# Performance work log

Hardware: AMD Instinct MI355X
Metric: run time of the kernel (lower is better)

The kernel has to match this reference:

```python
import jax, jax.numpy as jnp
import numpy as np

B, N, D = 1, 1024, 3584
H, KVH, HD = 28, 4, 128
I = 18944
SEC = [16, 24, 24]  # mrope_section, sums to HD//2
EPS_RMS = 1e-6
EPS_SM = 1e-6


def setup_inputs() -> dict:
    key = jax.random.key(0)
    ks = jax.random.split(key, 16)
    s = 0.02
    return {
        "hidden_states": jax.random.normal(ks[0], (B, N, D), jnp.float32),
        "cos": jax.random.uniform(ks[1], (3, B, N, HD), jnp.float32, -1.0, 1.0),
        "sin": jax.random.uniform(ks[2], (3, B, N, HD), jnp.float32, -1.0, 1.0),
        "prune_mask": jax.random.randint(ks[3], (B, N), 0, 2, jnp.int32),
        "Wq": jax.random.normal(ks[4], (D, H * HD), jnp.float32) * s,
        "bq": jnp.zeros((H * HD,), jnp.float32),
        "Wk": jax.random.normal(ks[5], (D, KVH * HD), jnp.float32) * s,
        "bk": jnp.zeros((KVH * HD,), jnp.float32),
        "Wv": jax.random.normal(ks[6], (D, KVH * HD), jnp.float32) * s,
        "bv": jnp.zeros((KVH * HD,), jnp.float32),
        "Wo": jax.random.normal(ks[7], (H * HD, D), jnp.float32) * s,
        "ln1_w": jnp.ones((D,), jnp.float32),
        "ln2_w": jnp.ones((D,), jnp.float32),
        "Wg": jax.random.normal(ks[8], (D, I), jnp.float32) * s,
        "Wu": jax.random.normal(ks[9], (D, I), jnp.float32) * s,
        "Wd": jax.random.normal(ks[10], (I, D), jnp.float32) * s,
    }


def _rmsnorm(x, w):
    v = jnp.mean(x * x, axis=-1, keepdims=True)
    return x * jax.lax.rsqrt(v + EPS_RMS) * w


def _rotate_half(x):
    h = x.shape[-1] // 2
    return jnp.concatenate([-x[..., h:], x[..., :h]], axis=-1)


def _mrope_select(t):
    # t: (3, B, N, HD) -> (B, 1, N, HD), picking section i from axis i%3
    parts, idx = [], 0
    for i, s in enumerate(SEC * 2):
        parts.append(t[i % 3, :, :, idx:idx + s])
        idx += s
    return jnp.concatenate(parts, axis=-1)[:, None]


def reference(hidden_states, cos, sin, prune_mask, Wq, bq, Wk, bk, Wv, bv, Wo,
              ln1_w, ln2_w, Wg, Wu, Wd):
    x = _rmsnorm(hidden_states, ln1_w)
    q = (x @ Wq + bq).reshape(B, N, H, HD).transpose(0, 2, 1, 3)
    k = (x @ Wk + bk).reshape(B, N, KVH, HD).transpose(0, 2, 1, 3)
    v = (x @ Wv + bv).reshape(B, N, KVH, HD).transpose(0, 2, 1, 3)

    cf, sf = _mrope_select(cos), _mrope_select(sin)
    q = q * cf + _rotate_half(q) * sf
    k = k * cf + _rotate_half(k) * sf

    groups = H // KVH
    k = jnp.repeat(k, groups, axis=1)  # (B,H,N,HD)
    v = jnp.repeat(v, groups, axis=1)

    scores = jnp.einsum("bhqd,bhkd->bhqk", q, k) / np.sqrt(HD).astype(np.float32)
    causal = jnp.tril(jnp.ones((N, N), bool))
    scores = jnp.where(causal, scores, jnp.float32(-1e9))

    # custom prune-masked softmax (softmax_with_mask)
    am = prune_mask.astype(jnp.float32)[:, None, None, :]  # (B,1,1,N)
    eye = jnp.eye(N, dtype=jnp.float32)
    am = am + (1.0 - am) * eye
    mx = jnp.max(scores, axis=-1, keepdims=True)
    e = jnp.exp(scores - mx) * am
    attn = (e + EPS_SM / N) / (jnp.sum(e, axis=-1, keepdims=True) + EPS_SM)

    o = jnp.einsum("bhqk,bhkd->bhqd", attn, v)
    o = o.transpose(0, 2, 1, 3).reshape(B, N, H * HD) @ Wo

    h = hidden_states + o
    y = _rmsnorm(h, ln2_w)
    mlp = (jax.nn.silu(y @ Wg) * (y @ Wu)) @ Wd
    return h + mlp
```

## Files before the change

### kernel.cpp

```cpp
#include <hip/hip_runtime.h>
#include <hip/hip_bf16.h>


#define SEQ   1024
#define DIM   3584
#define NH    28
#define NKVH  4
#define HDIM  128
#define IDIM  18944
#define QKVN  4608
#define GUN   37888

typedef __attribute__((ext_vector_type(8))) __bf16 bf16x8;
typedef __attribute__((ext_vector_type(4))) __bf16 bf16x4;
typedef __attribute__((ext_vector_type(4))) float  f32x4;

static constexpr size_t OFF_WQKVT = 0;
static constexpr size_t OFF_WOT   = OFF_WQKVT + (size_t)QKVN*DIM*2;
static constexpr size_t OFF_WGUT  = OFF_WOT   + (size_t)DIM*DIM*2;
static constexpr size_t OFF_WDT   = OFF_WGUT  + (size_t)GUN*DIM*2;
static constexpr size_t OFF_XB    = OFF_WDT   + (size_t)DIM*IDIM*2;
static constexpr size_t OFF_QKV   = OFF_XB    + (size_t)SEQ*DIM*2;
static constexpr size_t OFF_VT    = OFF_QKV   + (size_t)SEQ*QKVN*2;
static constexpr size_t OFF_VSUMP = OFF_VT    + (size_t)NKVH*HDIM*SEQ*2;
static constexpr size_t OFF_VSUM  = OFF_VSUMP + 4*8*128*4;
static constexpr size_t OFF_BQKV  = OFF_VSUM  + 4*128*4;
static constexpr size_t OFF_OB    = OFF_BQKV  + (size_t)QKVN*4;
static constexpr size_t OFF_HB    = OFF_OB    + (size_t)SEQ*DIM*2;
static constexpr size_t OFF_YB    = OFF_HB    + (size_t)SEQ*DIM*4;
static constexpr size_t OFF_GU    = OFF_YB    + (size_t)SEQ*DIM*2;
static constexpr size_t OFF_PB    = OFF_GU    + (size_t)SEQ*GUN*2;
static constexpr size_t OFF_PART  = OFF_GU;
static constexpr size_t OFF_CTR   = OFF_VSUMP;

#define GLL16(gp, lp)                                                        \
  __builtin_amdgcn_global_load_lds(                                         \
      (const __attribute__((address_space(1))) void*)(gp),                  \
      (__attribute__((address_space(3))) void*)(lp), 16, 0, 0)

#define BAR    asm volatile("s_barrier" ::: "memory")
#define LGKM0  asm volatile("s_waitcnt lgkmcnt(0)" ::: "memory")
#define VM4    asm volatile("s_waitcnt vmcnt(4)" ::: "memory")

__global__ __launch_bounds__(256) void transconv_kernel(
    const float* __restrict__ W, __bf16* __restrict__ WT, int K, int N, int mode)
{
  __shared__ __bf16 t[64][72];
  const int tid = threadIdx.x;
  const int k0 = blockIdx.y * 64, n0 = blockIdx.x * 64;
#pragma unroll
  for (int it = 0; it < 4; ++it) {
    int idx = it * 256 + tid;
    int r = idx >> 4, c4 = idx & 15;
    float4 v = *(const float4*)(W + (size_t)(k0 + r) * N + n0 + c4 * 4);
    t[r][c4 * 4 + 0] = (__bf16)v.x;
    t[r][c4 * 4 + 1] = (__bf16)v.y;
    t[r][c4 * 4 + 2] = (__bf16)v.z;
    t[r][c4 * 4 + 3] = (__bf16)v.w;
  }
  __syncthreads();
#pragma unroll
  for (int it = 0; it < 2; ++it) {
    int idx = it * 256 + tid;
    int r = idx >> 3, c8 = idx & 7;
    bf16x8 o;
#pragma unroll
    for (int i = 0; i < 8; ++i) o[i] = t[c8 * 8 + i][r];
    const int nlog = n0 + r;
    const int orow = (mode == 0) ? nlog
                   : ((nlog >> 4) << 5) + ((mode == 2) ? 16 : 0) + (nlog & 15);
    *(bf16x8*)(WT + (size_t)orow * K + k0 + c8 * 8) = o;
  }
}

__global__ __launch_bounds__(256) void pack_bias_kernel(
    const float* __restrict__ bq, const float* __restrict__ bk,
    const float* __restrict__ bv, float* __restrict__ out)
{
  int i = blockIdx.x * 256 + threadIdx.x;
  if (i < DIM) out[i] = bq[i];
  else if (i < DIM + 512) out[i] = bk[i - DIM];
  else if (i < QKVN) out[i] = bv[i - DIM - 512];
}

__global__ __launch_bounds__(256) void rmsnorm_kernel(
    const float* __restrict__ in, const float* __restrict__ w,
    __bf16* __restrict__ out)
{
  const int row = blockIdx.x;
  const int t = threadIdx.x;
  const float* x = in + (size_t)row * DIM;
  float4 v[4];
  float ss = 0.f;
#pragma unroll
  for (int i = 0; i < 4; ++i) {
    int idx = t + i * 256;
    if (idx < 896) {
      v[i] = ((const float4*)x)[idx];
      ss += v[i].x * v[i].x + v[i].y * v[i].y + v[i].z * v[i].z + v[i].w * v[i].w;
    }
  }
#pragma unroll
  for (int m = 1; m < 64; m <<= 1) ss += __shfl_xor(ss, m);
  __shared__ float red[4];
  if ((t & 63) == 0) red[t >> 6] = ss;
  __syncthreads();
  float tot = red[0] + red[1] + red[2] + red[3];
  float rs = rsqrtf(tot / (float)DIM + 1e-6f);
#pragma unroll
  for (int i = 0; i < 4; ++i) {
    int idx = t + i * 256;
    if (idx < 896) {
      float4 wv = ((const float4*)w)[idx];
      bf16x4 o;
      o[0] = (__bf16)(v[i].x * rs * wv.x);
      o[1] = (__bf16)(v[i].y * rs * wv.y);
      o[2] = (__bf16)(v[i].z * rs * wv.z);
      o[3] = (__bf16)(v[i].w * rs * wv.w);
      *(bf16x4*)(out + (size_t)row * DIM + idx * 4) = o;
    }
  }
}

template<int S, bool BF16OUT, bool BIAS>
__global__ __launch_bounds__(256) void reduce_kernel(
    const float* __restrict__ part, const float* __restrict__ resid,
    const float* __restrict__ bias, void* __restrict__ out, int N, int MN4)
{
  const int i4 = blockIdx.x * 256 + threadIdx.x;
  if (i4 >= MN4) return;
  const size_t base = (size_t)i4 * 4;
  f32x4 s = *(const f32x4*)(part + base);
#pragma unroll
  for (int k = 1; k < S; ++k)
    s += *(const f32x4*)(part + (size_t)k * MN4 * 4 + base);
  if (BIAS) {
    const int col = (int)(base % N);
    s += *(const f32x4*)(bias + col);
  }
  if (resid != nullptr) s += *(const f32x4*)(resid + base);
  if (BF16OUT) {
    bf16x4 o;
#pragma unroll
    for (int j = 0; j < 4; ++j) o[j] = (__bf16)s[j];
    *(bf16x4*)((__bf16*)out + base) = o;
  } else {
    *(f32x4*)((float*)out + base) = s;
  }
}

__global__ __launch_bounds__(256) void reduce_rms_kernel(
    const float* __restrict__ part, const float* __restrict__ resid,
    const float* __restrict__ w, float* __restrict__ hout,
    __bf16* __restrict__ yout, int* __restrict__ ctr)
{
  const int row = blockIdx.x;
  const int t = threadIdx.x;
  if (row == 0 && t == 0) atomicExch(ctr, 0);
  const size_t base = (size_t)row * DIM;
  const size_t slab = (size_t)SEQ * DIM;
  f32x4 v[4];
  float ss = 0.f;
#pragma unroll
  for (int i = 0; i < 4; ++i) {
    int idx = t + i * 256;
    if (idx < 896) {
      f32x4 s = *(const f32x4*)(part + base + idx * 4);
      s += *(const f32x4*)(part + slab + base + idx * 4);
      s += *(const f32x4*)(part + 2 * slab + base + idx * 4);
      s += *(const f32x4*)(part + 3 * slab + base + idx * 4);
      s += *(const f32x4*)(resid + base + idx * 4);
      v[i] = s;
      ss += s[0] * s[0] + s[1] * s[1] + s[2] * s[2] + s[3] * s[3];
      *(f32x4*)(hout + base + idx * 4) = s;
    }
  }
#pragma unroll
  for (int m = 1; m < 64; m <<= 1) ss += __shfl_xor(ss, m);
  __shared__ float red[4];
  if ((t & 63) == 0) red[t >> 6] = ss;
  __syncthreads();
  float tot = red[0] + red[1] + red[2] + red[3];
  float rs = rsqrtf(tot / (float)DIM + 1e-6f);
#pragma unroll
  for (int i = 0; i < 4; ++i) {
    int idx = t + i * 256;
    if (idx < 896) {
      f32x4 wv = *(const f32x4*)(w + idx * 4);
      bf16x4 o;
#pragma unroll
      for (int j = 0; j < 4; ++j) o[j] = (__bf16)(v[i][j] * rs * wv[j]);
      *(bf16x4*)(yout + base + idx * 4) = o;
    }
  }
}

template<int EPI, int PERSIST>
__global__ __launch_bounds__(512, 1) void gemm256_kernel(
    const __bf16* __restrict__ A, const __bf16* __restrict__ BT,
    void* __restrict__ OUT, int M, int N, int K, int Kc, int gridY,
    int NT, int* __restrict__ ctr)
{
  __shared__ int4 lds4[8192];
  __shared__ int s_t;
  char* ldsc = (char*)lds4;
  const int tid = threadIdx.x;
  const int l = tid & 63, w = tid >> 6;
  const int wr = w >> 2, wc = w & 3;
  const int lg = l >> 4, lc = l & 15;

  int cdst[2], crow[2], cslot[2];
#pragma unroll
  for (int j = 0; j < 2; ++j) {
    const int c = (j * 8 + w) * 64 + l;
    crow[j] = c >> 3;
    cslot[j] = (c & 7) ^ (crow[j] & 7);
    cdst[j] = (j * 8 + w) * 1024;
  }
  const int sw = lc & 7;
  const int rdA = (wr * 128 + lc) * 128;
  const int rdB = 32768 + (wc * 64 + lc) * 128;
  const int sk0 = (lg ^ sw) * 16;
  const int sk1 = ((4 | lg) ^ sw) * 16;
  const int ntn = N >> 8;

  for (;;) {
    int tw;
    if (PERSIST) {
      if (tid == 0) s_t = atomicAdd(ctr, 1);
      __syncthreads();
      tw = s_t;
      if (tw >= NT) return;
    } else {
      const int nwg = gridDim.x;
      const int bq8 = nwg >> 3, br8 = nwg & 7;
      const int xcd = blockIdx.x & 7, bidx = blockIdx.x >> 3;
      tw = (xcd < br8 ? xcd * (bq8 + 1) : br8 * (bq8 + 1) + (xcd - br8) * bq8) + bidx;
    }
    const int wg2 = tw / gridY;
    const int row0 = (tw % gridY) * 256;
    const int col0 = (wg2 % ntn) * 256;
    const int ks_ = wg2 / ntn;
    const int kbase = ks_ * Kc;

    size_t aoffj[2], boffj[2];
    int dstj[2];
#pragma unroll
    for (int j = 0; j < 2; ++j) {
      aoffj[j] = (size_t)(row0 + crow[j]) * K + kbase + cslot[j] * 8;
      boffj[j] = (size_t)(col0 + crow[j]) * K + kbase + cslot[j] * 8;
      dstj[j] = cdst[j];
    }

#define STG_A(U, KT, BUFB) do {                                              \
    GLL16(A + aoffj[0] + (size_t)(U) * 128 * K + (size_t)(KT) * 64,          \
          ldsc + (BUFB) + (U) * 16384 + dstj[0]);                            \
    GLL16(A + aoffj[1] + (size_t)(U) * 128 * K + (size_t)(KT) * 64,          \
          ldsc + (BUFB) + (U) * 16384 + dstj[1]); } while (0)
#define STG_B(U, KT, BUFB) do {                                              \
    GLL16(BT + boffj[0] + (size_t)(U) * 128 * K + (size_t)(KT) * 64,         \
          ldsc + (BUFB) + 32768 + (U) * 16384 + dstj[0]);                    \
    GLL16(BT + boffj[1] + (size_t)(U) * 128 * K + (size_t)(KT) * 64,         \
          ldsc + (BUFB) + 32768 + (U) * 16384 + dstj[1]); } while (0)

    f32x4 acc[8][4] = {};
    bf16x8 af[4][2], bfr[4][2];

#define RD_A4(MH, BUFB) do { _Pragma("unroll")                               \
    for (int mm = 0; mm < 4; ++mm) {                                         \
      af[mm][0] = *(const bf16x8*)(ldsc + (BUFB) + rdA + ((MH) * 4 + mm) * 2048 + sk0); \
      af[mm][1] = *(const bf16x8*)(ldsc + (BUFB) + rdA + ((MH) * 4 + mm) * 2048 + sk1); } } while (0)
#define RD_B2(NL, BUFB) do { _Pragma("unroll")                               \
    for (int nn = 0; nn < 2; ++nn) {                                         \
      bfr[(NL) + nn][0] = *(const bf16x8*)(ldsc + (BUFB) + rdB + ((NL) + nn) * 2048 + sk0); \
      bfr[(NL) + nn][1] = *(const bf16x8*)(ldsc + (BUFB) + rdB + ((NL) + nn) * 2048 + sk1); } } while (0)

#define MFMA16(MH, NL) do { _Pragma("unroll")                                \
    for (int mm = 0; mm < 4; ++mm) { _Pragma("unroll")                       \
      for (int nn = 0; nn < 2; ++nn) {                                       \
        acc[(MH)*4+mm][(NL)+nn] = __builtin_amdgcn_mfma_f32_16x16x32_bf16(   \
            af[mm][0], bfr[(NL)+nn][0], acc[(MH)*4+mm][(NL)+nn], 0, 0, 0);   \
        acc[(MH)*4+mm][(NL)+nn] = __builtin_amdgcn_mfma_f32_16x16x32_bf16(   \
            af[mm][1], bfr[(NL)+nn][1], acc[(MH)*4+mm][(NL)+nn], 0, 0, 0); } } } while (0)

#define DO_MFMA(MH, NL)                                                      \
    __builtin_amdgcn_s_setprio(1); MFMA16(MH, NL);                           \
    __builtin_amdgcn_s_setprio(0)

    STG_B(0, 0, 0); STG_B(1, 0, 0); STG_A(0, 0, 0); STG_A(1, 0, 0);
    STG_B(0, 1, 65536); STG_B(1, 1, 65536);
    VM4;
    BAR;

    const int T = Kc >> 6;
#pragma unroll 1
    for (int i = 0; i < (T >> 1); ++i) {
      const int t1 = 2 * i + 1;
      const int se = (2 * i + 2 < T) ? 2 * i + 2 : 2 * i;
      const int so = (2 * i + 3 < T) ? 2 * i + 3 : t1;
      RD_A4(0, 0); RD_B2(0, 0); STG_A(0, t1, 65536);
      BAR; LGKM0; DO_MFMA(0, 0); BAR;
      RD_B2(2, 0); STG_A(1, t1, 65536);
      BAR; LGKM0; DO_MFMA(0, 2); BAR;
      RD_A4(1, 0); STG_B(0, se, 0);
      BAR; LGKM0; DO_MFMA(1, 2); BAR;
      STG_B(1, se, 0);
      VM4;
      BAR; DO_MFMA(1, 0); BAR;
      RD_A4(0, 65536); RD_B2(0, 65536); STG_A(0, se, 0);
      BAR; LGKM0; DO_MFMA(0, 0); BAR;
      RD_B2(2, 65536); STG_A(1, se, 0);
      BAR; LGKM0; DO_MFMA(0, 2); BAR;
      RD_A4(1, 65536); STG_B(0, so, 65536);
      BAR; LGKM0; DO_MFMA(1, 2); BAR;
      STG_B(1, so, 65536);
      VM4;
      BAR; DO_MFMA(1, 0); BAR;
    }
    asm volatile("s_waitcnt vmcnt(0)" ::: "memory");

    if (EPI == 0) {
      __bf16* PBo = (__bf16*)OUT;
      const int id = N >> 1;
      const int baseq = (col0 + wc * 64) >> 5;
#pragma unroll
      for (int m = 0; m < 8; ++m) {
#pragma unroll
        for (int p = 0; p < 2; ++p) {
          const int gcol = (baseq + p) * 16 + lc;
#pragma unroll
          for (int j = 0; j < 4; ++j) {
            const int row = row0 + wr * 128 + m * 16 + lg * 4 + j;
            const float g = acc[m][2 * p][j];
            const float u = acc[m][2 * p + 1][j];
            const float s = g / (1.f + __expf(-g));
            PBo[(size_t)row * id + gcol] = (__bf16)(s * u);
          }
        }
      }
    } else {
      float* P = (float*)OUT + (size_t)ks_ * M * N;
#pragma unroll
      for (int m = 0; m < 8; ++m)
#pragma unroll
        for (int n = 0; n < 4; ++n)
#pragma unroll
          for (int j = 0; j < 4; ++j)
            P[(size_t)(row0 + wr * 128 + m * 16 + lg * 4 + j) * N
              + (col0 + wc * 64 + n * 16 + lc)] = acc[m][n][j];
    }
    if (!PERSIST) return;
  }
#undef STG_A
#undef STG_B
#undef RD_A4
#undef RD_B2
#undef MFMA16
#undef DO_MFMA
}

__global__ __launch_bounds__(256) void rope_kernel(
    __bf16* __restrict__ qkv, const float* __restrict__ cosb,
    const float* __restrict__ sinb)
{
  const int n = blockIdx.x;
  for (int p = threadIdx.x; p < 32 * 64; p += 256) {
    const int head = p >> 6;
    const int d = p & 63;
    const int src = (d < 16) ? 0 : (d < 40) ? 1 : 2;
    const float* cb = cosb + (size_t)src * SEQ * HDIM + (size_t)n * HDIM;
    const float* sb = sinb + (size_t)src * SEQ * HDIM + (size_t)n * HDIM;
    const float c0 = cb[d], c1 = cb[d + 64];
    const float s0 = sb[d], s1 = sb[d + 64];
    const int col = (head < NH) ? head * HDIM : DIM + (head - NH) * HDIM;
    __bf16* q = qkv + (size_t)n * QKVN + col;
    const float a = (float)q[d];
    const float b = (float)q[d + 64];
    q[d]      = (__bf16)(a * c0 - b * s0);
    q[d + 64] = (__bf16)(b * c1 + a * s1);
  }
}

__global__ __launch_bounds__(256) void vtrans_kernel(
    const __bf16* __restrict__ qkv, __bf16* __restrict__ vT,
    float* __restrict__ vsump)
{
  __shared__ __bf16 t[128][132];
  const int nt = blockIdx.x, kvh = blockIdx.y;
  const int n0 = nt * 128;
  const int tid = threadIdx.x;
#pragma unroll
  for (int it = 0; it < 8; ++it) {
    int idx = it * 256 + tid;
    int nl = idx >> 4, c8 = idx & 15;
    bf16x8 v = *(const bf16x8*)(qkv + (size_t)(n0 + nl) * QKVN + 4096 + kvh * HDIM + c8 * 8);
#pragma unroll
    for (int i = 0; i < 8; ++i) t[nl][c8 * 8 + i] = v[i];
  }
  __syncthreads();
#pragma unroll
  for (int it = 0; it < 8; ++it) {
    int idx = it * 256 + tid;
    int d = idx >> 4, c8 = idx & 15;
    bf16x8 o;
#pragma unroll
    for (int i = 0; i < 8; ++i) o[i] = t[c8 * 8 + i][d];
    *(bf16x8*)(vT + (size_t)(kvh * HDIM + d) * SEQ + n0 + c8 * 8) = o;
  }
  if (tid < 128) {
    float s = 0.f;
    for (int nl = 0; nl < 128; ++nl) s += (float)t[nl][tid];
    vsump[(size_t)(kvh * 8 + nt) * 128 + tid] = s;
  }
}

__global__ __launch_bounds__(512) void vsum_reduce_kernel(
    const float* __restrict__ vsump, float* __restrict__ vsum)
{
  const int idx = threadIdx.x;
  const int kvh = idx >> 7, d = idx & 127;
  float s = 0.f;
#pragma unroll
  for (int nt = 0; nt < 8; ++nt) s += vsump[(size_t)(kvh * 8 + nt) * 128 + d];
  vsum[idx] = s;
}

__global__ __launch_bounds__(256) void attn_kernel(
    const __bf16* __restrict__ qkv, const __bf16* __restrict__ vT,
    const float* __restrict__ vsum, const int* __restrict__ prune,
    __bf16* __restrict__ o)
{
  __shared__ __bf16 plds[4 * 16 * 40];
  const int tid = threadIdx.x;
  const int l = tid & 63, w = tid >> 6;
  const int h = blockIdx.y;
  const int kvh = h / 7;
  const int qt = blockIdx.x;
  const int qbase = qt * 64 + w * 16;
  const int lg = l >> 4, lc = l & 15;
  __bf16* pw = plds + w * (16 * 40);

  bf16x8 qf[4];
#pragma unroll
  for (int s = 0; s < 4; ++s)
    qf[s] = *(const bf16x8*)(qkv + (size_t)(qbase + lc) * QKVN + h * HDIM + s * 32 + lg * 8);

  f32x4 oacc[8] = {};
  float mrun[4] = {-3e38f, -3e38f, -3e38f, -3e38f};
  float lrun[4] = {0.f, 0.f, 0.f, 0.f};

  const int kbEnd = ((qbase + 15) >> 5) + 1;
  for (int kb = 0; kb < kbEnd; ++kb) {
    f32x4 sacc[2] = {};
#pragma unroll
    for (int s = 0; s < 4; ++s) {
#pragma unroll
      for (int c = 0; c < 2; ++c) {
        bf16x8 kf = *(const bf16x8*)(qkv + (size_t)(kb * 32 + c * 16 + lc) * QKVN
                                     + DIM + kvh * HDIM + s * 32 + lg * 8);
        sacc[c] = __builtin_amdgcn_mfma_f32_16x16x32_bf16(qf[s], kf, sacc[c], 0, 0, 0);
      }
    }
    float p[2][4];
    int am[2];
#pragma unroll
    for (int c = 0; c < 2; ++c) {
      const int col = kb * 32 + c * 16 + lc;
      am[c] = (prune[col] != 0) ? 1 : 0;
#pragma unroll
      for (int j = 0; j < 4; ++j) {
        const int row = qbase + lg * 4 + j;
        float sv = sacc[c][j] * 0.08838834764831845f;
        p[c][j] = (col <= row) ? sv : -3e38f;
      }
    }
#pragma unroll
    for (int j = 0; j < 4; ++j) {
      float mx = fmaxf(p[0][j], p[1][j]);
      mx = fmaxf(mx, __shfl_xor(mx, 1));
      mx = fmaxf(mx, __shfl_xor(mx, 2));
      mx = fmaxf(mx, __shfl_xor(mx, 4));
      mx = fmaxf(mx, __shfl_xor(mx, 8));
      const float mnew = fmaxf(mrun[j], mx);
      const float scale = __expf(mrun[j] - mnew);
      mrun[j] = mnew;
      const int row = qbase + lg * 4 + j;
      float rs = 0.f;
#pragma unroll
      for (int c = 0; c < 2; ++c) {
        const int col = kb * 32 + c * 16 + lc;
        float e = __expf(p[c][j] - mnew);
        const int keep = (col == row) ? 1 : am[c];
        e = keep ? e : 0.f;
        p[c][j] = e;
        rs += e;
      }
      rs += __shfl_xor(rs, 1);
      rs += __shfl_xor(rs, 2);
      rs += __shfl_xor(rs, 4);
      rs += __shfl_xor(rs, 8);
      lrun[j] = lrun[j] * scale + rs;
#pragma unroll
      for (int df = 0; df < 8; ++df) oacc[df][j] *= scale;
    }
#pragma unroll
    for (int c = 0; c < 2; ++c)
#pragma unroll
      for (int j = 0; j < 4; ++j)
        pw[(lg * 4 + j) * 40 + c * 16 + lc] = (__bf16)p[c][j];
    bf16x8 pa = *(const bf16x8*)(pw + lc * 40 + lg * 8);
#pragma unroll
    for (int df = 0; df < 8; ++df) {
      bf16x8 vf = *(const bf16x8*)(vT + (size_t)(kvh * HDIM + df * 16 + lc) * SEQ + kb * 32 + lg * 8);
      oacc[df] = __builtin_amdgcn_mfma_f32_16x16x32_bf16(pa, vf, oacc[df], 0, 0, 0);
    }
  }
#pragma unroll
  for (int df = 0; df < 8; ++df) {
    const float vs = vsum[kvh * HDIM + df * 16 + lc];
#pragma unroll
    for (int j = 0; j < 4; ++j) {
      const int row = qbase + lg * 4 + j;
      const float denom = lrun[j] + 1e-6f;
      const float val = (oacc[df][j] + 9.765625e-10f * vs) / denom;
      o[(size_t)row * DIM + h * HDIM + df * 16 + lc] = (__bf16)val;
    }
  }
}

extern "C" void kernel_launch(void* const* d_in, const int* in_sizes, int n_in,
                              void* d_out, int out_size, void* d_ws, size_t ws_size,
                              hipStream_t stream) {
  const float* hidden = (const float*)d_in[0];
  const float* cosb   = (const float*)d_in[1];
  const float* sinb   = (const float*)d_in[2];
  const int*   prune  = (const int*)d_in[3];
  const float* Wq     = (const float*)d_in[4];
  const float* bq     = (const float*)d_in[5];
  const float* Wk     = (const float*)d_in[6];
  const float* bk     = (const float*)d_in[7];
  const float* Wv     = (const float*)d_in[8];
  const float* bv     = (const float*)d_in[9];
  const float* Wo     = (const float*)d_in[10];
  const float* ln1    = (const float*)d_in[11];
  const float* ln2    = (const float*)d_in[12];
  const float* Wg     = (const float*)d_in[13];
  const float* Wu     = (const float*)d_in[14];
  const float* Wd     = (const float*)d_in[15];
  float* out = (float*)d_out;
  char* ws = (char*)d_ws;

  __bf16* WQKVT = (__bf16*)(ws + OFF_WQKVT);
  __bf16* WOT   = (__bf16*)(ws + OFF_WOT);
  __bf16* WGUT  = (__bf16*)(ws + OFF_WGUT);
  __bf16* WDT   = (__bf16*)(ws + OFF_WDT);
  __bf16* XB    = (__bf16*)(ws + OFF_XB);
  __bf16* QKV   = (__bf16*)(ws + OFF_QKV);
  __bf16* VT    = (__bf16*)(ws + OFF_VT);
  float*  VSUMP = (float*)(ws + OFF_VSUMP);
  float*  VSUM  = (float*)(ws + OFF_VSUM);
  float*  BQKV  = (float*)(ws + OFF_BQKV);
  __bf16* OB    = (__bf16*)(ws + OFF_OB);
  float*  HB    = (float*)(ws + OFF_HB);
  __bf16* YB    = (__bf16*)(ws + OFF_YB);
  __bf16* PB    = (__bf16*)(ws + OFF_PB);
  float*  PART  = (float*)(ws + OFF_PART);
  int*    CTR   = (int*)(ws + OFF_CTR);

  transconv_kernel<<<dim3(DIM / 64, DIM / 64), 256, 0, stream>>>(Wq, WQKVT, DIM, DIM, 0);
  transconv_kernel<<<dim3(512 / 64, DIM / 64), 256, 0, stream>>>(Wk, WQKVT + (size_t)DIM * DIM, DIM, 512, 0);
  transconv_kernel<<<dim3(512 / 64, DIM / 64), 256, 0, stream>>>(Wv, WQKVT + (size_t)4096 * DIM, DIM, 512, 0);
  pack_bias_kernel<<<QKVN / 256, 256, 0, stream>>>(bq, bk, bv, BQKV);
  rmsnorm_kernel<<<SEQ, 256, 0, stream>>>(hidden, ln1, XB);

  gemm256_kernel<1, 0><<<(SEQ / 256) * (QKVN / 256) * 2, 512, 0, stream>>>(
      XB, WQKVT, PART, SEQ, QKVN, DIM, DIM / 2, SEQ / 256, 0, nullptr);
  reduce_kernel<2, true, true><<<(SEQ * QKVN / 4 + 255) / 256, 256, 0, stream>>>(
      PART, nullptr, BQKV, QKV, QKVN, SEQ * QKVN / 4);

  rope_kernel<<<SEQ, 256, 0, stream>>>(QKV, cosb, sinb);
  vtrans_kernel<<<dim3(8, NKVH), 256, 0, stream>>>(QKV, VT, VSUMP);
  vsum_reduce_kernel<<<1, 512, 0, stream>>>(VSUMP, VSUM);
  attn_kernel<<<dim3(SEQ / 64, NH), 256, 0, stream>>>(QKV, VT, VSUM, prune, OB);

  transconv_kernel<<<dim3(DIM / 64, DIM / 64), 256, 0, stream>>>(Wo, WOT, DIM, DIM, 0);
  gemm256_kernel<1, 0><<<(DIM / 256) * (SEQ / 256) * 4, 512, 0, stream>>>(
      OB, WOT, PART, SEQ, DIM, DIM, DIM / 4, SEQ / 256, 0, nullptr);
  reduce_rms_kernel<<<SEQ, 256, 0, stream>>>(PART, hidden, ln2, HB, YB, CTR);

  transconv_kernel<<<dim3(IDIM / 64, DIM / 64), 256, 0, stream>>>(Wg, WGUT, DIM, IDIM, 1);
  transconv_kernel<<<dim3(IDIM / 64, DIM / 64), 256, 0, stream>>>(Wu, WGUT, DIM, IDIM, 2);
  gemm256_kernel<0, 1><<<256, 512, 0, stream>>>(
      YB, WGUT, PB, SEQ, GUN, DIM, DIM, SEQ / 256,
      (GUN / 256) * (SEQ / 256), CTR);

  transconv_kernel<<<dim3(DIM / 64, IDIM / 64), 256, 0, stream>>>(Wd, WDT, IDIM, DIM, 0);
  gemm256_kernel<1, 0><<<(DIM / 256) * (SEQ / 256) * 4, 512, 0, stream>>>(
      PB, WDT, PART, SEQ, DIM, IDIM, IDIM / 4, SEQ / 256, 0, nullptr);
  reduce_kernel<4, false, false><<<(SEQ * DIM / 4 + 255) / 256, 256, 0, stream>>>(
      PART, HB, nullptr, out, DIM, SEQ * DIM / 4);
}
```

Before: 989.0 us.

## Fuse QKV split-K reduce with mRoPE and drop persistent gate/up GEMM

```diff
diff --git a/kernel.cpp b/kernel.cpp
--- a/kernel.cpp
+++ b/kernel.cpp
@@ -31,7 +31,6 @@
 static constexpr size_t OFF_GU    = OFF_YB    + (size_t)SEQ*DIM*2;
 static constexpr size_t OFF_PB    = OFF_GU    + (size_t)SEQ*GUN*2;
 static constexpr size_t OFF_PART  = OFF_GU;
-static constexpr size_t OFF_CTR   = OFF_VSUMP;
 
 #define GLL16(gp, lp)                                                        \
   __builtin_amdgcn_global_load_lds(                                         \
@@ -149,14 +148,67 @@
   }
 }
 
+__global__ __launch_bounds__(256) void qkv_reduce_rope_kernel(
+    const float* __restrict__ part, const float* __restrict__ bias,
+    const float* __restrict__ cosb, const float* __restrict__ sinb,
+    __bf16* __restrict__ qkv)
+{
+  const int n = blockIdx.x;
+  const int t = threadIdx.x;
+  const size_t rb = (size_t)n * QKVN;
+  const size_t slab = (size_t)SEQ * QKVN;
+
+  const int head = t >> 3;
+  const int d0 = (t & 7) * 8;
+  const int col = (head < NH) ? head * HDIM + d0 : DIM + (head - NH) * HDIM + d0;
+
+  float lo[8], hi[8];
+#pragma unroll
+  for (int j = 0; j < 8; j += 4) {
+    f32x4 a  = *(const f32x4*)(part + rb + col + j);
+    f32x4 b  = *(const f32x4*)(part + slab + rb + col + j);
+    f32x4 bi = *(const f32x4*)(bias + col + j);
+    f32x4 a2  = *(const f32x4*)(part + rb + col + 64 + j);
+    f32x4 b2  = *(const f32x4*)(part + slab + rb + col + 64 + j);
+    f32x4 bi2 = *(const f32x4*)(bias + col + 64 + j);
+#pragma unroll
+    for (int i = 0; i < 4; ++i) {
+      lo[j + i] = a[i] + b[i] + bi[i];
+      hi[j + i] = a2[i] + b2[i] + bi2[i];
+    }
+  }
+  bf16x8 olo, ohi;
+#pragma unroll
+  for (int j = 0; j < 8; ++j) {
+    const int d = d0 + j;
+    const int src = (d < 16) ? 0 : (d < 40) ? 1 : 2;
+    const float* cb = cosb + ((size_t)src * SEQ + n) * HDIM;
+    const float* sb = sinb + ((size_t)src * SEQ + n) * HDIM;
+    const float c0 = cb[d], s0 = sb[d];
+    const float c1 = cb[d + 64], s1 = sb[d + 64];
+    olo[j] = (__bf16)(lo[j] * c0 - hi[j] * s0);
+    ohi[j] = (__bf16)(hi[j] * c1 + lo[j] * s1);
+  }
+  *(bf16x8*)(qkv + rb + col) = olo;
+  *(bf16x8*)(qkv + rb + col + 64) = ohi;
+
+  {
+    const int vc = 4096 + t * 2;
+    float2 a  = *(const float2*)(part + rb + vc);
+    float2 b  = *(const float2*)(part + slab + rb + vc);
+    float2 bi = *(const float2*)(bias + vc);
+    qkv[rb + vc]     = (__bf16)(a.x + b.x + bi.x);
+    qkv[rb + vc + 1] = (__bf16)(a.y + b.y + bi.y);
+  }
+}
+
 __global__ __launch_bounds__(256) void reduce_rms_kernel(
     const float* __restrict__ part, const float* __restrict__ resid,
     const float* __restrict__ w, float* __restrict__ hout,
-    __bf16* __restrict__ yout, int* __restrict__ ctr)
+    __bf16* __restrict__ yout)
 {
   const int row = blockIdx.x;
   const int t = threadIdx.x;
-  if (row == 0 && t == 0) atomicExch(ctr, 0);
   const size_t base = (size_t)row * DIM;
   const size_t slab = (size_t)SEQ * DIM;
   f32x4 v[4];
@@ -195,62 +247,40 @@
   }
 }
 
-template<int EPI, int PERSIST>
+template<int EPI>
 __global__ __launch_bounds__(512, 1) void gemm256_kernel(
     const __bf16* __restrict__ A, const __bf16* __restrict__ BT,
-    void* __restrict__ OUT, int M, int N, int K, int Kc, int gridY,
-    int NT, int* __restrict__ ctr)
+    void* __restrict__ OUT, int M, int N, int K, int Kc, int gridY)
 {
   __shared__ int4 lds4[8192];
-  __shared__ int s_t;
   char* ldsc = (char*)lds4;
   const int tid = threadIdx.x;
   const int l = tid & 63, w = tid >> 6;
   const int wr = w >> 2, wc = w & 3;
   const int lg = l >> 4, lc = l & 15;
 
-  int cdst[2], crow[2], cslot[2];
+  const int nwg = gridDim.x;
+  const int bq8 = nwg >> 3, br8 = nwg & 7;
+  const int xcd = blockIdx.x & 7, bidx = blockIdx.x >> 3;
+  const int wg = (xcd < br8 ? xcd * (bq8 + 1) : br8 * (bq8 + 1) + (xcd - br8) * bq8) + bidx;
+  const int ntn = N >> 8;
+  const int wg2 = wg / gridY;
+  const int row0 = (wg % gridY) * 256;
+  const int col0 = (wg2 % ntn) * 256;
+  const int ks_ = wg2 / ntn;
+  const int kbase = ks_ * Kc;
+
+  size_t aoffj[2], boffj[2];
+  int dstj[2];
 #pragma unroll
   for (int j = 0; j < 2; ++j) {
     const int c = (j * 8 + w) * 64 + l;
-    crow[j] = c >> 3;
-    cslot[j] = (c & 7) ^ (crow[j] & 7);
-    cdst[j] = (j * 8 + w) * 1024;
-  }
-  const int sw = lc & 7;
-  const int rdA = (wr * 128 + lc) * 128;
-  const int rdB = 32768 + (wc * 64 + lc) * 128;
-  const int sk0 = (lg ^ sw) * 16;
-  const int sk1 = ((4 | lg) ^ sw) * 16;
-  const int ntn = N >> 8;
-
-  for (;;) {
-    int tw;
-    if (PERSIST) {
-      if (tid == 0) s_t = atomicAdd(ctr, 1);
-      __syncthreads();
-      tw = s_t;
-      if (tw >= NT) return;
-    } else {
-      const int nwg = gridDim.x;
-      const int bq8 = nwg >> 3, br8 = nwg & 7;
-      const int xcd = blockIdx.x & 7, bidx = blockIdx.x >> 3;
-      tw = (xcd < br8 ? xcd * (bq8 + 1) : br8 * (bq8 + 1) + (xcd - br8) * bq8) + bidx;
-    }
-    const int wg2 = tw / gridY;
-    const int row0 = (tw % gridY) * 256;
-    const int col0 = (wg2 % ntn) * 256;
-    const int ks_ = wg2 / ntn;
-    const int kbase = ks_ * Kc;
-
-    size_t aoffj[2], boffj[2];
-    int dstj[2];
-#pragma unroll
-    for (int j = 0; j < 2; ++j) {
-      aoffj[j] = (size_t)(row0 + crow[j]) * K + kbase + cslot[j] * 8;
-      boffj[j] = (size_t)(col0 + crow[j]) * K + kbase + cslot[j] * 8;
-      dstj[j] = cdst[j];
-    }
+    const int r = c >> 3, p = c & 7;
+    const int b = p ^ (r & 7);
+    aoffj[j] = (size_t)(row0 + r) * K + kbase + b * 8;
+    boffj[j] = (size_t)(col0 + r) * K + kbase + b * 8;
+    dstj[j] = (j * 8 + w) * 1024;
+  }
 
 #define STG_A(U, KT, BUFB) do {                                              \
     GLL16(A + aoffj[0] + (size_t)(U) * 128 * K + (size_t)(KT) * 64,          \
@@ -263,8 +293,14 @@
     GLL16(BT + boffj[1] + (size_t)(U) * 128 * K + (size_t)(KT) * 64,         \
           ldsc + (BUFB) + 32768 + (U) * 16384 + dstj[1]); } while (0)
 
-    f32x4 acc[8][4] = {};
-    bf16x8 af[4][2], bfr[4][2];
+  const int sw = lc & 7;
+  const int rdA = (wr * 128 + lc) * 128;
+  const int rdB = 32768 + (wc * 64 + lc) * 128;
+  const int sk0 = (lg ^ sw) * 16;
+  const int sk1 = ((4 | lg) ^ sw) * 16;
+
+  f32x4 acc[8][4] = {};
+  bf16x8 af[4][2], bfr[4][2];
 
 #define RD_A4(MH, BUFB) do { _Pragma("unroll")                               \
     for (int mm = 0; mm < 4; ++mm) {                                         \
@@ -287,69 +323,67 @@
     __builtin_amdgcn_s_setprio(1); MFMA16(MH, NL);                           \
     __builtin_amdgcn_s_setprio(0)
 
-    STG_B(0, 0, 0); STG_B(1, 0, 0); STG_A(0, 0, 0); STG_A(1, 0, 0);
-    STG_B(0, 1, 65536); STG_B(1, 1, 65536);
+  STG_B(0, 0, 0); STG_B(1, 0, 0); STG_A(0, 0, 0); STG_A(1, 0, 0);
+  STG_B(0, 1, 65536); STG_B(1, 1, 65536);
+  VM4;
+  BAR;
+
+  const int T = Kc >> 6;
+#pragma unroll 1
+  for (int i = 0; i < (T >> 1); ++i) {
+    const int t1 = 2 * i + 1;
+    const int se = (2 * i + 2 < T) ? 2 * i + 2 : 2 * i;
+    const int so = (2 * i + 3 < T) ? 2 * i + 3 : t1;
+    RD_A4(0, 0); RD_B2(0, 0); STG_A(0, t1, 65536);
+    BAR; LGKM0; DO_MFMA(0, 0); BAR;
+    RD_B2(2, 0); STG_A(1, t1, 65536);
+    BAR; LGKM0; DO_MFMA(0, 2); BAR;
+    RD_A4(1, 0); STG_B(0, se, 0);
+    BAR; LGKM0; DO_MFMA(1, 2); BAR;
+    STG_B(1, se, 0);
     VM4;
-    BAR;
-
-    const int T = Kc >> 6;
-#pragma unroll 1
-    for (int i = 0; i < (T >> 1); ++i) {
-      const int t1 = 2 * i + 1;
-      const int se = (2 * i + 2 < T) ? 2 * i + 2 : 2 * i;
-      const int so = (2 * i + 3 < T) ? 2 * i + 3 : t1;
-      RD_A4(0, 0); RD_B2(0, 0); STG_A(0, t1, 65536);
-      BAR; LGKM0; DO_MFMA(0, 0); BAR;
-      RD_B2(2, 0); STG_A(1, t1, 65536);
-      BAR; LGKM0; DO_MFMA(0, 2); BAR;
-      RD_A4(1, 0); STG_B(0, se, 0);
-      BAR; LGKM0; DO_MFMA(1, 2); BAR;
-      STG_B(1, se, 0);
-      VM4;
-      BAR; DO_MFMA(1, 0); BAR;
-      RD_A4(0, 65536); RD_B2(0, 65536); STG_A(0, se, 0);
-      BAR; LGKM0; DO_MFMA(0, 0); BAR;
-      RD_B2(2, 65536); STG_A(1, se, 0);
-      BAR; LGKM0; DO_MFMA(0, 2); BAR;
-      RD_A4(1, 65536); STG_B(0, so, 65536);
-      BAR; LGKM0; DO_MFMA(1, 2); BAR;
-      STG_B(1, so, 65536);
-      VM4;
-      BAR; DO_MFMA(1, 0); BAR;
-    }
-    asm volatile("s_waitcnt vmcnt(0)" ::: "memory");
-
-    if (EPI == 0) {
-      __bf16* PBo = (__bf16*)OUT;
-      const int id = N >> 1;
-      const int baseq = (col0 + wc * 64) >> 5;
-#pragma unroll
-      for (int m = 0; m < 8; ++m) {
-#pragma unroll
-        for (int p = 0; p < 2; ++p) {
-          const int gcol = (baseq + p) * 16 + lc;
-#pragma unroll
-          for (int j = 0; j < 4; ++j) {
-            const int row = row0 + wr * 128 + m * 16 + lg * 4 + j;
-            const float g = acc[m][2 * p][j];
-            const float u = acc[m][2 * p + 1][j];
-            const float s = g / (1.f + __expf(-g));
-            PBo[(size_t)row * id + gcol] = (__bf16)(s * u);
-          }
+    BAR; DO_MFMA(1, 0); BAR;
+    RD_A4(0, 65536); RD_B2(0, 65536); STG_A(0, se, 0);
+    BAR; LGKM0; DO_MFMA(0, 0); BAR;
+    RD_B2(2, 65536); STG_A(1, se, 0);
+    BAR; LGKM0; DO_MFMA(0, 2); BAR;
+    RD_A4(1, 65536); STG_B(0, so, 65536);
+    BAR; LGKM0; DO_MFMA(1, 2); BAR;
+    STG_B(1, so, 65536);
+    VM4;
+    BAR; DO_MFMA(1, 0); BAR;
+  }
+  asm volatile("s_waitcnt vmcnt(0)" ::: "memory");
+
+  if (EPI == 0) {
+    __bf16* PBo = (__bf16*)OUT;
+    const int id = N >> 1;
+    const int baseq = (col0 + wc * 64) >> 5;
+#pragma unroll
+    for (int m = 0; m < 8; ++m) {
+#pragma unroll
+      for (int p = 0; p < 2; ++p) {
+        const int gcol = (baseq + p) * 16 + lc;
+#pragma unroll
+        for (int j = 0; j < 4; ++j) {
+          const int row = row0 + wr * 128 + m * 16 + lg * 4 + j;
+          const float g = acc[m][2 * p][j];
+          const float u = acc[m][2 * p + 1][j];
+          const float s = g / (1.f + __expf(-g));
+          PBo[(size_t)row * id + gcol] = (__bf16)(s * u);
         }
       }
-    } else {
-      float* P = (float*)OUT + (size_t)ks_ * M * N;
-#pragma unroll
-      for (int m = 0; m < 8; ++m)
-#pragma unroll
-        for (int n = 0; n < 4; ++n)
-#pragma unroll
-          for (int j = 0; j < 4; ++j)
-            P[(size_t)(row0 + wr * 128 + m * 16 + lg * 4 + j) * N
-              + (col0 + wc * 64 + n * 16 + lc)] = acc[m][n][j];
-    }
-    if (!PERSIST) return;
+    }
+  } else {
+    float* P = (float*)OUT + (size_t)ks_ * M * N;
+#pragma unroll
+    for (int m = 0; m < 8; ++m)
+#pragma unroll
+      for (int n = 0; n < 4; ++n)
+#pragma unroll
+        for (int j = 0; j < 4; ++j)
+          P[(size_t)(row0 + wr * 128 + m * 16 + lg * 4 + j) * N
+            + (col0 + wc * 64 + n * 16 + lc)] = acc[m][n][j];
   }
 #undef STG_A
 #undef STG_B
@@ -357,28 +391,6 @@
 #undef RD_B2
 #undef MFMA16
 #undef DO_MFMA
-}
-
-__global__ __launch_bounds__(256) void rope_kernel(
-    __bf16* __restrict__ qkv, const float* __restrict__ cosb,
-    const float* __restrict__ sinb)
-{
-  const int n = blockIdx.x;
-  for (int p = threadIdx.x; p < 32 * 64; p += 256) {
-    const int head = p >> 6;
-    const int d = p & 63;
-    const int src = (d < 16) ? 0 : (d < 40) ? 1 : 2;
-    const float* cb = cosb + (size_t)src * SEQ * HDIM + (size_t)n * HDIM;
-    const float* sb = sinb + (size_t)src * SEQ * HDIM + (size_t)n * HDIM;
-    const float c0 = cb[d], c1 = cb[d + 64];
-    const float s0 = sb[d], s1 = sb[d + 64];
-    const int col = (head < NH) ? head * HDIM : DIM + (head - NH) * HDIM;
-    __bf16* q = qkv + (size_t)n * QKVN + col;
-    const float a = (float)q[d];
-    const float b = (float)q[d + 64];
-    q[d]      = (__bf16)(a * c0 - b * s0);
-    q[d + 64] = (__bf16)(b * c1 + a * s1);
-  }
 }
 
 __global__ __launch_bounds__(256) void vtrans_kernel(
@@ -565,7 +577,6 @@
   __bf16* YB    = (__bf16*)(ws + OFF_YB);
   __bf16* PB    = (__bf16*)(ws + OFF_PB);
   float*  PART  = (float*)(ws + OFF_PART);
-  int*    CTR   = (int*)(ws + OFF_CTR);
 
   transconv_kernel<<<dim3(DIM / 64, DIM / 64), 256, 0, stream>>>(Wq, WQKVT, DIM, DIM, 0);
   transconv_kernel<<<dim3(512 / 64, DIM / 64), 256, 0, stream>>>(Wk, WQKVT + (size_t)DIM * DIM, DIM, 512, 0);
@@ -573,30 +584,27 @@
   pack_bias_kernel<<<QKVN / 256, 256, 0, stream>>>(bq, bk, bv, BQKV);
   rmsnorm_kernel<<<SEQ, 256, 0, stream>>>(hidden, ln1, XB);
 
-  gemm256_kernel<1, 0><<<(SEQ / 256) * (QKVN / 256) * 2, 512, 0, stream>>>(
-      XB, WQKVT, PART, SEQ, QKVN, DIM, DIM / 2, SEQ / 256, 0, nullptr);
-  reduce_kernel<2, true, true><<<(SEQ * QKVN / 4 + 255) / 256, 256, 0, stream>>>(
-      PART, nullptr, BQKV, QKV, QKVN, SEQ * QKVN / 4);
-
-  rope_kernel<<<SEQ, 256, 0, stream>>>(QKV, cosb, sinb);
+  gemm256_kernel<1><<<(SEQ / 256) * (QKVN / 256) * 2, 512, 0, stream>>>(
+      XB, WQKVT, PART, SEQ, QKVN, DIM, DIM / 2, SEQ / 256);
+  qkv_reduce_rope_kernel<<<SEQ, 256, 0, stream>>>(PART, BQKV, cosb, sinb, QKV);
+
   vtrans_kernel<<<dim3(8, NKVH), 256, 0, stream>>>(QKV, VT, VSUMP);
   vsum_reduce_kernel<<<1, 512, 0, stream>>>(VSUMP, VSUM);
   attn_kernel<<<dim3(SEQ / 64, NH), 256, 0, stream>>>(QKV, VT, VSUM, prune, OB);
 
   transconv_kernel<<<dim3(DIM / 64, DIM / 64), 256, 0, stream>>>(Wo, WOT, DIM, DIM, 0);
-  gemm256_kernel<1, 0><<<(DIM / 256) * (SEQ / 256) * 4, 512, 0, stream>>>(
-      OB, WOT, PART, SEQ, DIM, DIM, DIM / 4, SEQ / 256, 0, nullptr);
-  reduce_rms_kernel<<<SEQ, 256, 0, stream>>>(PART, hidden, ln2, HB, YB, CTR);
+  gemm256_kernel<1><<<(DIM / 256) * (SEQ / 256) * 4, 512, 0, stream>>>(
+      OB, WOT, PART, SEQ, DIM, DIM, DIM / 4, SEQ / 256);
+  reduce_rms_kernel<<<SEQ, 256, 0, stream>>>(PART, hidden, ln2, HB, YB);
 
   transconv_kernel<<<dim3(IDIM / 64, DIM / 64), 256, 0, stream>>>(Wg, WGUT, DIM, IDIM, 1);
   transconv_kernel<<<dim3(IDIM / 64, DIM / 64), 256, 0, stream>>>(Wu, WGUT, DIM, IDIM, 2);
-  gemm256_kernel<0, 1><<<256, 512, 0, stream>>>(
-      YB, WGUT, PB, SEQ, GUN, DIM, DIM, SEQ / 256,
-      (GUN / 256) * (SEQ / 256), CTR);
+  gemm256_kernel<0><<<(GUN / 256) * (SEQ / 256), 512, 0, stream>>>(
+      YB, WGUT, PB, SEQ, GUN, DIM, DIM, SEQ / 256);
 
   transconv_kernel<<<dim3(DIM / 64, IDIM / 64), 256, 0, stream>>>(Wd, WDT, IDIM, DIM, 0);
-  gemm256_kernel<1, 0><<<(DIM / 256) * (SEQ / 256) * 4, 512, 0, stream>>>(
-      PB, WDT, PART, SEQ, DIM, IDIM, IDIM / 4, SEQ / 256, 0, nullptr);
+  gemm256_kernel<1><<<(DIM / 256) * (SEQ / 256) * 4, 512, 0, stream>>>(
+      PB, WDT, PART, SEQ, DIM, IDIM, IDIM / 4, SEQ / 256);
   reduce_kernel<4, false, false><<<(SEQ * DIM / 4 + 255) / 256, 256, 0, stream>>>(
       PART, HB, nullptr, out, DIM, SEQ * DIM / 4);
 }
```

Result: faster. 929.4 us (-6.0%).
